# Performance work log

Hardware: AMD Instinct MI355X
Metric: run time of the kernel (lower is better)

Reference implementation:

```python
import jax, jax.numpy as jnp
import numpy as np

K_POOL = 5

def _conv_lookahead(x, W):
    # Faithful to F.conv2d(pad=(fs//2+1,0)) followed by keeping the last L rows:
    # for fs=3 this reduces to out[t] = sum_j x[t+j] @ W[:,j,:].T (2 trailing zeros).
    # x: [..., L, E], W: [nf, fs, E] -> out [..., L, nf]
    fs = W.shape[1]
    L = x.shape[-2]
    pad = [(0, 0)] * (x.ndim - 2) + [(0, fs - 1), (0, 0)]
    xp = jnp.pad(x, pad)
    out = sum(jnp.einsum('...le,fe->...lf', jax.lax.dynamic_slice_in_dim(xp, j, L, axis=-2), W[:, j, :]) for j in range(fs))
    return out

def _cosine(q, s):
    # q: [B,Q,D], s: [B,S,L,D] -> [B,S,Q,L]
    num = jnp.einsum('bqd,bsld->bsql', q, s)
    qn = jnp.linalg.norm(q, axis=-1)  # [B,Q]
    sn = jnp.linalg.norm(s, axis=-1)  # [B,S,L]
    return num / (qn[:, None, :, None] * sn[:, :, None, :])

def _pool(sim, k=K_POOL):
    # sort-based k-max pooling over last dim -> (max, mean-of-top-k), matching torch.sort + slice
    top = jax.lax.top_k(sim, k)[0]            # [..., Q, k] descending
    return jnp.stack([top[..., 0], top.mean(-1)], axis=-1)  # [..., Q, 2]

def _bce(p, t):
    return -(t * jnp.log(p) + (1.0 - t) * jnp.log(1.0 - p)).mean()

def setup_inputs() -> dict:
    key = jax.random.key(0)
    ks = jax.random.split(key, 9)
    B, S, L, Q, V, E, NF, FS = 16, 48, 64, 32, 50000, 300, 256, 3
    return {
        'sentences': jax.random.randint(ks[0], (B, S, L), 0, V, dtype=jnp.int64 if jax.config.jax_enable_x64 else jnp.int32).astype(jnp.int32),
        'question': jax.random.randint(ks[1], (B, Q), 0, V).astype(jnp.int32),
        'target_sents': jax.random.randint(ks[2], (B, S), 0, 2).astype(jnp.int32),
        'target_docs': jax.random.randint(ks[3], (B,), 0, 2).astype(jnp.int32),
        'similarity_one_hot': jax.random.uniform(ks[4], (B, S, Q, L), dtype=jnp.float32),
        'embeds': jax.random.normal(ks[5], (V, E), dtype=jnp.float32),
        'conv_w': jax.random.normal(ks[6], (NF, FS, E), dtype=jnp.float32),
        'lin_w': jax.random.normal(ks[7], (1, 6), dtype=jnp.float32),
        'lin_b': jax.random.normal(ks[8], (1,), dtype=jnp.float32),
    }

def reference(sentences, question, target_sents, target_docs, similarity_one_hot, embeds, conv_w, lin_w, lin_b):
    q_emb = embeds[question]            # [B,Q,E]
    s_emb = embeds[sentences]           # [B,S,L,E]
    q_conv = _conv_lookahead(q_emb, conv_w)   # [B,Q,NF]
    s_conv = _conv_lookahead(s_emb, conv_w)   # [B,S,L,NF]

    sim_ins = _cosine(q_emb, s_emb)     # [B,S,Q,L]
    qmask = (question > 1).astype(sim_ins.dtype)   # [B,Q]
    smask = (sentences > 1).astype(sim_ins.dtype)  # [B,S,L]
    sim_ins = sim_ins * qmask[:, None, :, None] * smask[:, :, None, :]

    sim_sens = _cosine(q_conv, s_conv)  # [B,S,Q,L]

    feats = jnp.concatenate([_pool(sim_ins), _pool(sim_sens), _pool(similarity_one_hot)], axis=-1)  # [B,S,Q,6]
    lo = jax.nn.sigmoid(jnp.einsum('bsqf,of->bsqo', feats, lin_w)[..., 0] + lin_b[0])  # [B,S,Q]
    sent_output = lo.mean(-1)           # [B,S]

    sal = _bce(sent_output, target_sents.astype(sent_output.dtype))
    doc_emit = sent_output.max(-1)      # [B]
    dal = _bce(doc_emit, target_docs.astype(doc_emit.dtype))
    total_loss = (sal + dal) / 2.0
    return (total_loss, sent_output, doc_emit)
```

## Files before the change

kernel.cpp:

```cpp
#include <hip/hip_runtime.h>
#include <math.h>

#define NB 16
#define NS 48
#define NL 64
#define NQ 32
#define NE 300
#define NF 256
#define KP 320
#define QROWS 36

typedef __attribute__((ext_vector_type(8))) short short8;
typedef __attribute__((ext_vector_type(4))) float f32x4;

#define MFMA(a,b,c) __builtin_amdgcn_mfma_f32_16x16x32_bf16((a),(b),(c),0,0,0)

__device__ __forceinline__ unsigned short f2bf(float f) {
    unsigned u = __float_as_uint(f);
    u += 0x7fff + ((u >> 16) & 1);
    return (unsigned short)(u >> 16);
}

#define SE_PITCH 640
#define SC_PITCH 512
#define SIM_OFF (66 * 640)
#define SIM_PITCH 66
#define DYN_LDS (SIM_OFF + NQ * SIM_PITCH * 4)

__device__ __forceinline__ float wave_reduce_sum(float v) {
#pragma unroll
    for (int off = 32; off; off >>= 1) v += __shfl_xor(v, off, 64);
    return v;
}

__device__ __forceinline__ void top5_pool4(float v0, float v1, float v2, float v3,
                                           int lane, float* mx, float* mn) {
    float s0 = 0.f, s1 = 0.f, s2 = 0.f, s3 = 0.f;
    float x0 = 0.f, x1 = 0.f, x2 = 0.f, x3 = 0.f;
#pragma unroll
    for (int i = 0; i < 5; ++i) {
        float m0 = v0, m1 = v1, m2 = v2, m3 = v3;
#pragma unroll
        for (int off = 32; off; off >>= 1) {
            m0 = fmaxf(m0, __shfl_xor(m0, off, 64));
            m1 = fmaxf(m1, __shfl_xor(m1, off, 64));
            m2 = fmaxf(m2, __shfl_xor(m2, off, 64));
            m3 = fmaxf(m3, __shfl_xor(m3, off, 64));
        }
        if (i == 0) { x0 = m0; x1 = m1; x2 = m2; x3 = m3; }
        s0 += m0; s1 += m1; s2 += m2; s3 += m3;
        unsigned long long k0 = __ballot(v0 == m0);
        unsigned long long k1 = __ballot(v1 == m1);
        unsigned long long k2 = __ballot(v2 == m2);
        unsigned long long k3 = __ballot(v3 == m3);
        if (lane == __ffsll(k0) - 1) v0 = -3.4e38f;
        if (lane == __ffsll(k1) - 1) v1 = -3.4e38f;
        if (lane == __ffsll(k2) - 1) v2 = -3.4e38f;
        if (lane == __ffsll(k3) - 1) v3 = -3.4e38f;
    }
    mx[0] = x0; mx[1] = x1; mx[2] = x2; mx[3] = x3;
    mn[0] = s0 * 0.2f; mn[1] = s1 * 0.2f; mn[2] = s2 * 0.2f; mn[3] = s3 * 0.2f;
}

__global__ void wb2_kernel(const float* __restrict__ conv_w, short8* __restrict__ Wb2,
                           unsigned int* __restrict__ done_ctr) {
    if (blockIdx.x == 0 && threadIdx.x == 0) done_ctr[0] = 0u;
    int i = blockIdx.x * 256 + threadIdx.x;
    if (i >= 120 * 256) return;
    int rl = i & 15;
    int ftile = (i >> 4) & 15;
    int c = i >> 8;
    int kg = c & 3, rest = c >> 2;
    int ks = rest % 10, j = rest / 10;
    int f = ftile * 16 + rl;
    int k0 = ks * 32 + kg * 8;
    const float* src = conv_w + (size_t)(f * 3 + j) * NE;
    short8 h;
#pragma unroll
    for (int e = 0; e < 8; ++e) {
        int k = k0 + e;
        h[e] = (short)((k < NE) ? f2bf(src[k]) : (unsigned short)0);
    }
    Wb2[i] = h;
}

__global__ void qe_kernel(const int* __restrict__ question, const float* __restrict__ embeds,
                          unsigned short* __restrict__ qe, short8* __restrict__ qef,
                          float* __restrict__ q_norm) {
    int row = blockIdx.x;
    int b = row / QROWS, r = row % QROWS;
    int l = threadIdx.x;
    unsigned short* dst = qe + (size_t)row * KP;
    if (r < NQ) {
        int tok = question[b * NQ + r];
        const float4* rp = (const float4*)(embeds + (size_t)tok * NE);
        short8 h = {0, 0, 0, 0, 0, 0, 0, 0};
        float ss = 0.f;
        if (l < 38) {
            float4 v0 = rp[2 * l];
            ss += v0.x * v0.x + v0.y * v0.y + v0.z * v0.z + v0.w * v0.w;
            h[0] = (short)f2bf(v0.x); h[1] = (short)f2bf(v0.y);
            h[2] = (short)f2bf(v0.z); h[3] = (short)f2bf(v0.w);
            if (2 * l + 1 < 75) {
                float4 v1 = rp[2 * l + 1];
                ss += v1.x * v1.x + v1.y * v1.y + v1.z * v1.z + v1.w * v1.w;
                h[4] = (short)f2bf(v1.x); h[5] = (short)f2bf(v1.y);
                h[6] = (short)f2bf(v1.z); h[7] = (short)f2bf(v1.w);
            }
        }
        if (l < 40) {
            *(short8*)(dst + 8 * l) = h;
            qef[((size_t)(b * 2 + (r >> 4)) * 40 + l) * 16 + (r & 15)] = h;
        }
        ss = wave_reduce_sum(ss);
        if (l == 0) q_norm[b * NQ + r] = sqrtf(ss);
    } else {
        if (l < 40) {
            short8 z = {0, 0, 0, 0, 0, 0, 0, 0};
            *(short8*)(dst + 8 * l) = z;
        }
    }
}

__global__ __launch_bounds__(256) void qconv_mfma_kernel(
        const unsigned short* __restrict__ qe, const short8* __restrict__ Wb2,
        short8* __restrict__ qcf) {
    __shared__ unsigned short tile[NQ][72];
    int b = blockIdx.x >> 2, fq = blockIdx.x & 3;
    int tid = threadIdx.x, lane = tid & 63, w = tid >> 6;
    int rl = lane & 15, kg = lane >> 4;
    int ftile = fq * 4 + w;
    f32x4 acc0 = (f32x4){0.f, 0.f, 0.f, 0.f};
    f32x4 acc1 = (f32x4){0.f, 0.f, 0.f, 0.f};
    for (int j = 0; j < 3; ++j) {
#pragma unroll 2
        for (int ks = 0; ks < 10; ++ks) {
            int k = ks * 32 + kg * 8;
            int c = (j * 10 + ks) * 4 + kg;
            short8 a0 = *(const short8*)(qe + ((size_t)(b * QROWS) + rl + j) * KP + k);
            short8 a1 = *(const short8*)(qe + ((size_t)(b * QROWS) + 16 + rl + j) * KP + k);
            short8 bb = Wb2[(c * 16 + ftile) * 16 + rl];
            acc0 = MFMA(a0, bb, acc0);
            acc1 = MFMA(a1, bb, acc1);
        }
    }
    int fl = w * 16 + rl;
#pragma unroll
    for (int reg = 0; reg < 4; ++reg) {
        tile[kg * 4 + reg][fl] = f2bf(acc0[reg]);
        tile[16 + kg * 4 + reg][fl] = f2bf(acc1[reg]);
    }
    __syncthreads();
    int mh = tid >> 7, c_local = (tid >> 4) & 7, rl2 = tid & 15;
    short8 h = *(const short8*)(&tile[mh * 16 + rl2][c_local * 8]);
    qcf[((size_t)(b * 2 + mh) * 32 + 8 * fq + c_local) * 16 + rl2] = h;
}

__global__ __launch_bounds__(256) void qcn_kernel(const short8* __restrict__ qcf,
                                                  float* __restrict__ qc_norm) {
    __shared__ float part[2][16][8];
    int b = blockIdx.x;
    int tid = threadIdx.x;
    int mh = tid >> 7, sub = (tid >> 4) & 7, rl = tid & 15;
    const short8* base = qcf + ((size_t)(b * 2 + mh) * 32) * 16;
    float ss = 0.f;
#pragma unroll
    for (int i = 0; i < 4; ++i) {
        short8 h = base[(sub * 4 + i) * 16 + rl];
#pragma unroll
        for (int e = 0; e < 8; ++e) {
            float v = __uint_as_float(((unsigned)(unsigned short)h[e]) << 16);
            ss += v * v;
        }
    }
    part[mh][rl][sub] = ss;
    __syncthreads();
    if (tid < 32) {
        int m2 = tid >> 4, r2 = tid & 15;
        float s = 0.f;
#pragma unroll
        for (int k = 0; k < 8; ++k) s += part[m2][r2][k];
        qc_norm[b * NQ + m2 * 16 + r2] = sqrtf(s);
    }
}

extern __shared__ char ldsc[];
__global__ __launch_bounds__(256, 3) void fused6_kernel(
    const int* __restrict__ sentences, const int* __restrict__ question,
    const float* __restrict__ sim_oh, const float* __restrict__ embeds,
    const short8* __restrict__ Wb2,
    const short8* __restrict__ qef, const short8* __restrict__ qcf,
    const float* __restrict__ q_norm, const float* __restrict__ qc_norm,
    const float* __restrict__ lin_w, const float* __restrict__ lin_b,
    const int* __restrict__ tsent, const int* __restrict__ tdoc,
    unsigned int* __restrict__ done_ctr,
    float* __restrict__ sent_ws, float* __restrict__ d_out)
{
    __shared__ int toks[NL];
    __shared__ float smaskf[NL], snorm[NL], scnorm[NL];
    __shared__ float qn_s[NQ], qcn_s[NQ], qmf_s[NQ];
    __shared__ float wq[4];
    __shared__ float fpool[NQ][2];
    __shared__ int lastflag;
    __shared__ float red2[4];
    __shared__ float dred[NB];

    int tid = threadIdx.x, lane = tid & 63, w = tid >> 6;
    int rl = lane & 15, kg = lane >> 4;
    int bs = blockIdx.x, b = bs / NS;
    int t = (w << 4) + rl, t7 = t & 7;

    if (tid < NL) {
        int tk = sentences[(size_t)bs * NL + tid];
        toks[tid] = tk;
        smaskf[tid] = (tk > 1) ? 1.f : 0.f;
    } else if (tid < NL + NQ) {
        int q = tid - NL;
        qn_s[q] = q_norm[b * NQ + q];
    } else if (tid < NL + 2 * NQ) {
        int q = tid - NL - NQ;
        qcn_s[q] = qc_norm[b * NQ + q];
    } else if (tid < NL + 3 * NQ) {
        int q = tid - NL - 2 * NQ;
        qmf_s[q] = (question[b * NQ + q] > 1) ? 1.f : 0.f;
    }
    __syncthreads();

#pragma unroll 2
    for (int r = w; r < 66; r += 4) {
        char* rowbase = ldsc + r * SE_PITCH;
        int m7 = r & 7;
        if (r < NL) {
            const float4* rp = (const float4*)(embeds + (size_t)toks[r] * NE);
            {
                float4 v = rp[lane];
                ushort4 h = {f2bf(v.x), f2bf(v.y), f2bf(v.z), f2bf(v.w)};
                *(ushort4*)(rowbase + (((lane >> 1) ^ m7) << 4) + ((lane & 1) << 3)) = h;
            }
            if (lane < 11) {
                float4 v = rp[64 + lane];
                ushort4 h = {f2bf(v.x), f2bf(v.y), f2bf(v.z), f2bf(v.w)};
                int g = 64 + lane;
                *(ushort4*)(rowbase + (((g >> 1) ^ m7) << 4) + ((g & 1) << 3)) = h;
            }
            if (lane < 5) {
                int pk = 37 + ((lane + 1) >> 1);
                int sub = ((lane + 1) & 1) << 3;
                *(unsigned long long*)(rowbase + ((pk ^ m7) << 4) + sub) = 0ull;
            }
        } else {
            if (lane < 40) {
                uint4 z = {0, 0, 0, 0};
                *(uint4*)(rowbase + (lane << 4)) = z;
            }
        }
    }
    __syncthreads();

    {
        f32x4 iacc0 = (f32x4){0.f, 0.f, 0.f, 0.f};
        f32x4 iacc1 = (f32x4){0.f, 0.f, 0.f, 0.f};
        f32x4 nB = (f32x4){0.f, 0.f, 0.f, 0.f};
        const short8* qf = qef + (size_t)(b * 80) * 16;
#pragma unroll 2
        for (int ks = 0; ks < 10; ++ks) {
            int c = ks * 4 + kg;
            short8 bB = *(const short8*)(ldsc + t * SE_PITCH + ((c ^ t7) << 4));
            short8 a0 = qf[c * 16 + rl];
            short8 a1 = qf[(40 + c) * 16 + rl];
            iacc0 = MFMA(a0, bB, iacc0);
            iacc1 = MFMA(a1, bB, iacc1);
            nB = MFMA(bB, bB, nB);
        }
        if (kg == (rl >> 2)) snorm[t] = sqrtf(nB[rl & 3]);
        __syncthreads();

        float inv_t = smaskf[t] / snorm[t];
#pragma unroll
        for (int reg = 0; reg < 4; ++reg) {
            int q0 = kg * 4 + reg;
            float s0 = iacc0[reg] / qn_s[q0] * inv_t * qmf_s[q0];
            *(float*)(ldsc + SIM_OFF + (q0 * SIM_PITCH + t) * 4) = s0;
            int q1 = 16 + kg * 4 + reg;
            float s1 = iacc1[reg] / qn_s[q1] * inv_t * qmf_s[q1];
            *(float*)(ldsc + SIM_OFF + (q1 * SIM_PITCH + t) * 4) = s1;
        }
    }
    __syncthreads();

    {
        int q0 = w << 3;
        float v[8];
#pragma unroll
        for (int qi = 0; qi < 8; ++qi)
            v[qi] = *(float*)(ldsc + SIM_OFF + ((q0 + qi) * SIM_PITCH + lane) * 4);
        float mx[4], mn[4];
        top5_pool4(v[0], v[1], v[2], v[3], lane, mx, mn);
        if (lane == 0)
#pragma unroll
            for (int p = 0; p < 4; ++p) { fpool[q0 + p][0] = mx[p]; fpool[q0 + p][1] = mn[p]; }
        top5_pool4(v[4], v[5], v[6], v[7], lane, mx, mn);
        if (lane == 0)
#pragma unroll
            for (int p = 0; p < 4; ++p) { fpool[q0 + 4 + p][0] = mx[p]; fpool[q0 + 4 + p][1] = mn[p]; }
    }

    f32x4 cacc[4][4];
#pragma unroll
    for (int m = 0; m < 4; ++m)
#pragma unroll
        for (int nn = 0; nn < 4; ++nn) cacc[m][nn] = (f32x4){0.f, 0.f, 0.f, 0.f};
    for (int j = 0; j < 3; ++j) {
#pragma unroll 2
        for (int ks = 0; ks < 10; ++ks) {
            int c = (j * 10 + ks) * 4 + kg;
            short8 a[4], bb[4];
#pragma unroll
            for (int m = 0; m < 4; ++m) {
                int row = m * 16 + rl + j;
                a[m] = *(const short8*)(ldsc + row * SE_PITCH +
                                        ((((ks << 2) + kg) ^ (row & 7)) << 4));
            }
#pragma unroll
            for (int nn = 0; nn < 4; ++nn)
                bb[nn] = Wb2[(c * 16 + (w * 4 + nn)) * 16 + rl];
#pragma unroll
            for (int m = 0; m < 4; ++m)
#pragma unroll
                for (int nn = 0; nn < 4; ++nn)
                    cacc[m][nn] = MFMA(a[m], bb[nn], cacc[m][nn]);
        }
    }
    __syncthreads();

#pragma unroll
    for (int m = 0; m < 4; ++m)
#pragma unroll
        for (int nn = 0; nn < 4; ++nn) {
            int f = (w * 4 + nn) * 16 + rl;
#pragma unroll
            for (int reg = 0; reg < 4; ++reg) {
                int tr = m * 16 + kg * 4 + reg;
                *(unsigned short*)(ldsc + tr * SC_PITCH +
                                   (((f >> 3) ^ (tr & 7)) << 4) + ((f & 7) << 1)) =
                    f2bf(cacc[m][nn][reg]);
            }
        }
    __syncthreads();

    float oh[8];
#pragma unroll
    for (int qi = 0; qi < 8; ++qi) {
        int q = (w << 3) + qi;
        oh[qi] = sim_oh[((size_t)bs * NQ + q) * NL + lane];
    }
    {
        f32x4 sacc0 = (f32x4){0.f, 0.f, 0.f, 0.f};
        f32x4 sacc1 = (f32x4){0.f, 0.f, 0.f, 0.f};
        f32x4 nB = (f32x4){0.f, 0.f, 0.f, 0.f};
        const short8* qc = qcf + (size_t)(b * 64) * 16;
#pragma unroll 2
        for (int ks = 0; ks < 8; ++ks) {
            int c = ks * 4 + kg;
            short8 bB = *(const short8*)(ldsc + t * SC_PITCH + ((c ^ t7) << 4));
            short8 a0 = qc[c * 16 + rl];
            short8 a1 = qc[(32 + c) * 16 + rl];
            sacc0 = MFMA(a0, bB, sacc0);
            sacc1 = MFMA(a1, bB, sacc1);
            nB = MFMA(bB, bB, nB);
        }
        if (kg == (rl >> 2)) scnorm[t] = sqrtf(nB[rl & 3]);
        __syncthreads();

        float inv_t = 1.f / scnorm[t];
#pragma unroll
        for (int reg = 0; reg < 4; ++reg) {
            int q0 = kg * 4 + reg;
            *(float*)(ldsc + SIM_OFF + (q0 * SIM_PITCH + t) * 4) =
                sacc0[reg] / qcn_s[q0] * inv_t;
            int q1 = 16 + kg * 4 + reg;
            *(float*)(ldsc + SIM_OFF + (q1 * SIM_PITCH + t) * 4) =
                sacc1[reg] / qcn_s[q1] * inv_t;
        }
    }
    __syncthreads();

    {
        float lw0 = lin_w[0], lw1 = lin_w[1], lw2 = lin_w[2];
        float lw3 = lin_w[3], lw4 = lin_w[4], lw5 = lin_w[5];
        float lb = lin_b[0];
        int q0 = w << 3;
        float sv[8];
#pragma unroll
        for (int qi = 0; qi < 8; ++qi)
            sv[qi] = *(float*)(ldsc + SIM_OFF + ((q0 + qi) * SIM_PITCH + lane) * 4);
        float mxs[8], mns[8], mxo[8], mno[8];
        top5_pool4(sv[0], sv[1], sv[2], sv[3], lane, mxs, mns);
        top5_pool4(sv[4], sv[5], sv[6], sv[7], lane, mxs + 4, mns + 4);
        top5_pool4(oh[0], oh[1], oh[2], oh[3], lane, mxo, mno);
        top5_pool4(oh[4], oh[5], oh[6], oh[7], lane, mxo + 4, mno + 4);
        float psum = 0.f;
#pragma unroll
        for (int qi = 0; qi < 8; ++qi) {
            float f0 = fpool[q0 + qi][0], f1 = fpool[q0 + qi][1];
            float z = f0 * lw0 + f1 * lw1 + mxs[qi] * lw2 + mns[qi] * lw3 +
                      mxo[qi] * lw4 + mno[qi] * lw5 + lb;
            psum += 1.f / (1.f + expf(-z));
        }
        if (lane == 0) wq[w] = psum;
    }
    __syncthreads();
    if (tid == 0) {
        float sent = (wq[0] + wq[1] + wq[2] + wq[3]) * (1.f / 32.f);
        __hip_atomic_store(&sent_ws[bs], sent, __ATOMIC_RELEASE, __HIP_MEMORY_SCOPE_AGENT);
        d_out[1 + bs] = sent;
        unsigned old = atomicAdd(done_ctr, 1u);
        lastflag = (old == (unsigned)(NB * NS - 1)) ? 1 : 0;
    }
    __syncthreads();

    if (lastflag) {
        float acc_l = 0.f;
        for (int i = tid; i < NB * NS; i += 256) {
            float p = __hip_atomic_load(&sent_ws[i], __ATOMIC_ACQUIRE, __HIP_MEMORY_SCOPE_AGENT);
            float tt2 = (float)tsent[i];
            acc_l += tt2 * logf(p) + (1.f - tt2) * logf(1.f - p);
        }
        acc_l = wave_reduce_sum(acc_l);
        if ((tid & 63) == 0) red2[tid >> 6] = acc_l;
        if (tid < NB) {
            float m = -3.4e38f;
            for (int s = 0; s < NS; ++s)
                m = fmaxf(m, __hip_atomic_load(&sent_ws[tid * NS + s], __ATOMIC_ACQUIRE,
                                               __HIP_MEMORY_SCOPE_AGENT));
            d_out[1 + NB * NS + tid] = m;
            float tt2 = (float)tdoc[tid];
            dred[tid] = tt2 * logf(m) + (1.f - tt2) * logf(1.f - m);
        }
        __syncthreads();
        if (tid == 0) {
            float sal = -(red2[0] + red2[1] + red2[2] + red2[3]) / (float)(NB * NS);
            float dsum = 0.f;
            for (int i = 0; i < NB; ++i) dsum += dred[i];
            float dal = -dsum / (float)NB;
            d_out[0] = 0.5f * (sal + dal);
        }
    }
}

extern "C" void kernel_launch(void* const* d_in, const int* in_sizes, int n_in,
                              void* d_out, int out_size, void* d_ws, size_t ws_size,
                              hipStream_t stream) {
    const int* sentences = (const int*)d_in[0];
    const int* question = (const int*)d_in[1];
    const int* tsent = (const int*)d_in[2];
    const int* tdoc = (const int*)d_in[3];
    const float* sim_oh = (const float*)d_in[4];
    const float* embeds = (const float*)d_in[5];
    const float* conv_w = (const float*)d_in[6];
    const float* lin_w = (const float*)d_in[7];
    const float* lin_b = (const float*)d_in[8];
    float* out = (float*)d_out;

    char* wsc = (char*)d_ws;
    short8* Wb2            = (short8*)(wsc);
    unsigned short* qe_old = (unsigned short*)(wsc + 491520);
    short8* qef            = (short8*)(wsc + 860160);
    short8* qcf            = (short8*)(wsc + 1187840);
    float* q_norm          = (float*)(wsc + 1449984);
    float* qc_norm         = (float*)(wsc + 1452032);
    float* sent_ws         = (float*)(wsc + 1454080);
    unsigned int* done_ctr = (unsigned int*)(wsc + 1457152);

    hipFuncSetAttribute(reinterpret_cast<const void*>(fused6_kernel),
                        hipFuncAttributeMaxDynamicSharedMemorySize, DYN_LDS);

    wb2_kernel<<<120, 256, 0, stream>>>(conv_w, Wb2, done_ctr);
    qe_kernel<<<NB * QROWS, 64, 0, stream>>>(question, embeds, qe_old, qef, q_norm);
    qconv_mfma_kernel<<<NB * 4, 256, 0, stream>>>(qe_old, Wb2, qcf);
    qcn_kernel<<<NB, 256, 0, stream>>>(qcf, qc_norm);
    fused6_kernel<<<NB * NS, 256, DYN_LDS, stream>>>(
        sentences, question, sim_oh, embeds, Wb2, qef, qcf, q_norm, qc_norm,
        lin_w, lin_b, tsent, tdoc, done_ctr, sent_ws, out);
}
```

Baseline: 130.6 us.

## Merge prep kernels, fold question-conv norms into atomics, hoist sim_oh loads

Merges the weight-conversion and question-embedding kernels into one prep launch and drops the separate question-conv norm kernel. The conv kernel now accumulates per-query sums of squares with atomics, and the main kernel takes the sqrt. The main kernel issues its sim_oh loads at the start so they overlap the embedding gather, and its row-staging loop is simplified to 16 unconditional iterations plus two zero rows. This cuts two kernel launches and the gaps between them, at the cost of atomic float accumulation order and higher register pressure from the early loads.

```diff
diff --git a/kernel.cpp b/kernel.cpp
--- a/kernel.cpp
+++ b/kernel.cpp
@@ -62,69 +62,73 @@
     mn[0] = s0 * 0.2f; mn[1] = s1 * 0.2f; mn[2] = s2 * 0.2f; mn[3] = s3 * 0.2f;
 }
 
-__global__ void wb2_kernel(const float* __restrict__ conv_w, short8* __restrict__ Wb2,
-                           unsigned int* __restrict__ done_ctr) {
-    if (blockIdx.x == 0 && threadIdx.x == 0) done_ctr[0] = 0u;
-    int i = blockIdx.x * 256 + threadIdx.x;
-    if (i >= 120 * 256) return;
-    int rl = i & 15;
-    int ftile = (i >> 4) & 15;
-    int c = i >> 8;
-    int kg = c & 3, rest = c >> 2;
-    int ks = rest % 10, j = rest / 10;
-    int f = ftile * 16 + rl;
-    int k0 = ks * 32 + kg * 8;
-    const float* src = conv_w + (size_t)(f * 3 + j) * NE;
-    short8 h;
-#pragma unroll
-    for (int e = 0; e < 8; ++e) {
-        int k = k0 + e;
-        h[e] = (short)((k < NE) ? f2bf(src[k]) : (unsigned short)0);
-    }
-    Wb2[i] = h;
-}
-
-__global__ void qe_kernel(const int* __restrict__ question, const float* __restrict__ embeds,
-                          unsigned short* __restrict__ qe, short8* __restrict__ qef,
-                          float* __restrict__ q_norm) {
-    int row = blockIdx.x;
-    int b = row / QROWS, r = row % QROWS;
-    int l = threadIdx.x;
-    unsigned short* dst = qe + (size_t)row * KP;
-    if (r < NQ) {
-        int tok = question[b * NQ + r];
-        const float4* rp = (const float4*)(embeds + (size_t)tok * NE);
-        short8 h = {0, 0, 0, 0, 0, 0, 0, 0};
-        float ss = 0.f;
-        if (l < 38) {
-            float4 v0 = rp[2 * l];
-            ss += v0.x * v0.x + v0.y * v0.y + v0.z * v0.z + v0.w * v0.w;
-            h[0] = (short)f2bf(v0.x); h[1] = (short)f2bf(v0.y);
-            h[2] = (short)f2bf(v0.z); h[3] = (short)f2bf(v0.w);
-            if (2 * l + 1 < 75) {
-                float4 v1 = rp[2 * l + 1];
-                ss += v1.x * v1.x + v1.y * v1.y + v1.z * v1.z + v1.w * v1.w;
-                h[4] = (short)f2bf(v1.x); h[5] = (short)f2bf(v1.y);
-                h[6] = (short)f2bf(v1.z); h[7] = (short)f2bf(v1.w);
+__global__ __launch_bounds__(256) void prep_kernel(
+        const float* __restrict__ conv_w, const int* __restrict__ question,
+        const float* __restrict__ embeds,
+        short8* __restrict__ Wb2, unsigned short* __restrict__ qe,
+        short8* __restrict__ qef, float* __restrict__ q_norm,
+        float* __restrict__ qcssq, unsigned int* __restrict__ done_ctr) {
+    int blk = blockIdx.x;
+    int tid = threadIdx.x;
+    if (blk < 120) {
+        if (blk == 0 && tid == 0) done_ctr[0] = 0u;
+        int i = blk * 256 + tid;
+        if (i < NB * NQ) qcssq[i] = 0.f;
+        int rl = i & 15;
+        int ftile = (i >> 4) & 15;
+        int c = i >> 8;
+        int kg = c & 3, rest = c >> 2;
+        int ks = rest % 10, j = rest / 10;
+        int f = ftile * 16 + rl;
+        int k0 = ks * 32 + kg * 8;
+        const float* src = conv_w + (size_t)(f * 3 + j) * NE;
+        short8 h;
+#pragma unroll
+        for (int e = 0; e < 8; ++e) {
+            int k = k0 + e;
+            h[e] = (short)((k < NE) ? f2bf(src[k]) : (unsigned short)0);
+        }
+        Wb2[i] = h;
+    } else {
+        int row = (blk - 120) * 4 + (tid >> 6);
+        int b = row / QROWS, r = row % QROWS;
+        int l = tid & 63;
+        unsigned short* dst = qe + (size_t)row * KP;
+        if (r < NQ) {
+            int tok = question[b * NQ + r];
+            const float4* rp = (const float4*)(embeds + (size_t)tok * NE);
+            short8 h = {0, 0, 0, 0, 0, 0, 0, 0};
+            float ss = 0.f;
+            if (l < 38) {
+                float4 v0 = rp[2 * l];
+                ss += v0.x * v0.x + v0.y * v0.y + v0.z * v0.z + v0.w * v0.w;
+                h[0] = (short)f2bf(v0.x); h[1] = (short)f2bf(v0.y);
+                h[2] = (short)f2bf(v0.z); h[3] = (short)f2bf(v0.w);
+                if (2 * l + 1 < 75) {
+                    float4 v1 = rp[2 * l + 1];
+                    ss += v1.x * v1.x + v1.y * v1.y + v1.z * v1.z + v1.w * v1.w;
+                    h[4] = (short)f2bf(v1.x); h[5] = (short)f2bf(v1.y);
+                    h[6] = (short)f2bf(v1.z); h[7] = (short)f2bf(v1.w);
+                }
             }
-        }
-        if (l < 40) {
-            *(short8*)(dst + 8 * l) = h;
-            qef[((size_t)(b * 2 + (r >> 4)) * 40 + l) * 16 + (r & 15)] = h;
-        }
-        ss = wave_reduce_sum(ss);
-        if (l == 0) q_norm[b * NQ + r] = sqrtf(ss);
-    } else {
-        if (l < 40) {
-            short8 z = {0, 0, 0, 0, 0, 0, 0, 0};
-            *(short8*)(dst + 8 * l) = z;
+            if (l < 40) {
+                *(short8*)(dst + 8 * l) = h;
+                qef[((size_t)(b * 2 + (r >> 4)) * 40 + l) * 16 + (r & 15)] = h;
+            }
+            ss = wave_reduce_sum(ss);
+            if (l == 0) q_norm[b * NQ + r] = sqrtf(ss);
+        } else {
+            if (l < 40) {
+                short8 z = {0, 0, 0, 0, 0, 0, 0, 0};
+                *(short8*)(dst + 8 * l) = z;
+            }
         }
     }
 }
 
 __global__ __launch_bounds__(256) void qconv_mfma_kernel(
         const unsigned short* __restrict__ qe, const short8* __restrict__ Wb2,
-        short8* __restrict__ qcf) {
+        short8* __restrict__ qcf, float* __restrict__ qcssq) {
     __shared__ unsigned short tile[NQ][72];
     int b = blockIdx.x >> 2, fq = blockIdx.x & 3;
     int tid = threadIdx.x, lane = tid & 63, w = tid >> 6;
@@ -151,46 +155,34 @@
         tile[16 + kg * 4 + reg][fl] = f2bf(acc1[reg]);
     }
     __syncthreads();
-    int mh = tid >> 7, c_local = (tid >> 4) & 7, rl2 = tid & 15;
-    short8 h = *(const short8*)(&tile[mh * 16 + rl2][c_local * 8]);
-    qcf[((size_t)(b * 2 + mh) * 32 + 8 * fq + c_local) * 16 + rl2] = h;
-}
-
-__global__ __launch_bounds__(256) void qcn_kernel(const short8* __restrict__ qcf,
-                                                  float* __restrict__ qc_norm) {
-    __shared__ float part[2][16][8];
-    int b = blockIdx.x;
-    int tid = threadIdx.x;
-    int mh = tid >> 7, sub = (tid >> 4) & 7, rl = tid & 15;
-    const short8* base = qcf + ((size_t)(b * 2 + mh) * 32) * 16;
-    float ss = 0.f;
-#pragma unroll
-    for (int i = 0; i < 4; ++i) {
-        short8 h = base[(sub * 4 + i) * 16 + rl];
+    {
+        int mh = tid >> 7, c_local = (tid >> 4) & 7, rl2 = tid & 15;
+        short8 h = *(const short8*)(&tile[mh * 16 + rl2][c_local * 8]);
+        qcf[((size_t)(b * 2 + mh) * 32 + 8 * fq + c_local) * 16 + rl2] = h;
+    }
+    {
+        int qq = tid >> 3, fgrp = tid & 7;
+        short8 h = *(const short8*)(&tile[qq][fgrp * 8]);
+        float ss = 0.f;
 #pragma unroll
         for (int e = 0; e < 8; ++e) {
             float v = __uint_as_float(((unsigned)(unsigned short)h[e]) << 16);
             ss += v * v;
         }
-    }
-    part[mh][rl][sub] = ss;
-    __syncthreads();
-    if (tid < 32) {
-        int m2 = tid >> 4, r2 = tid & 15;
-        float s = 0.f;
-#pragma unroll
-        for (int k = 0; k < 8; ++k) s += part[m2][r2][k];
-        qc_norm[b * NQ + m2 * 16 + r2] = sqrtf(s);
+        ss += __shfl_xor(ss, 1, 64);
+        ss += __shfl_xor(ss, 2, 64);
+        ss += __shfl_xor(ss, 4, 64);
+        if (fgrp == 0) atomicAdd(&qcssq[b * NQ + qq], ss);
     }
 }
 
 extern __shared__ char ldsc[];
-__global__ __launch_bounds__(256, 3) void fused6_kernel(
+__global__ __launch_bounds__(256, 3) void fused8_kernel(
     const int* __restrict__ sentences, const int* __restrict__ question,
     const float* __restrict__ sim_oh, const float* __restrict__ embeds,
     const short8* __restrict__ Wb2,
     const short8* __restrict__ qef, const short8* __restrict__ qcf,
-    const float* __restrict__ q_norm, const float* __restrict__ qc_norm,
+    const float* __restrict__ q_norm, const float* __restrict__ qcssq,
     const float* __restrict__ lin_w, const float* __restrict__ lin_b,
     const int* __restrict__ tsent, const int* __restrict__ tdoc,
     unsigned int* __restrict__ done_ctr,
@@ -210,6 +202,13 @@
     int bs = blockIdx.x, b = bs / NS;
     int t = (w << 4) + rl, t7 = t & 7;
 
+    float oh[8];
+#pragma unroll
+    for (int qi = 0; qi < 8; ++qi) {
+        int q = (w << 3) + qi;
+        oh[qi] = sim_oh[((size_t)bs * NQ + q) * NL + lane];
+    }
+
     if (tid < NL) {
         int tk = sentences[(size_t)bs * NL + tid];
         toks[tid] = tk;
@@ -219,40 +218,41 @@
         qn_s[q] = q_norm[b * NQ + q];
     } else if (tid < NL + 2 * NQ) {
         int q = tid - NL - NQ;
-        qcn_s[q] = qc_norm[b * NQ + q];
+        qcn_s[q] = sqrtf(qcssq[b * NQ + q]);
     } else if (tid < NL + 3 * NQ) {
         int q = tid - NL - 2 * NQ;
         qmf_s[q] = (question[b * NQ + q] > 1) ? 1.f : 0.f;
     }
     __syncthreads();
 
-#pragma unroll 2
-    for (int r = w; r < 66; r += 4) {
+#pragma unroll 4
+    for (int i = 0; i < 16; ++i) {
+        int r = (i << 2) + w;
         char* rowbase = ldsc + r * SE_PITCH;
         int m7 = r & 7;
-        if (r < NL) {
-            const float4* rp = (const float4*)(embeds + (size_t)toks[r] * NE);
-            {
-                float4 v = rp[lane];
-                ushort4 h = {f2bf(v.x), f2bf(v.y), f2bf(v.z), f2bf(v.w)};
-                *(ushort4*)(rowbase + (((lane >> 1) ^ m7) << 4) + ((lane & 1) << 3)) = h;
-            }
-            if (lane < 11) {
-                float4 v = rp[64 + lane];
-                ushort4 h = {f2bf(v.x), f2bf(v.y), f2bf(v.z), f2bf(v.w)};
-                int g = 64 + lane;
-                *(ushort4*)(rowbase + (((g >> 1) ^ m7) << 4) + ((g & 1) << 3)) = h;
-            }
-            if (lane < 5) {
-                int pk = 37 + ((lane + 1) >> 1);
-                int sub = ((lane + 1) & 1) << 3;
-                *(unsigned long long*)(rowbase + ((pk ^ m7) << 4) + sub) = 0ull;
-            }
-        } else {
-            if (lane < 40) {
-                uint4 z = {0, 0, 0, 0};
-                *(uint4*)(rowbase + (lane << 4)) = z;
-            }
+        const float4* rp = (const float4*)(embeds + (size_t)toks[r] * NE);
+        {
+            float4 v = rp[lane];
+            ushort4 h = {f2bf(v.x), f2bf(v.y), f2bf(v.z), f2bf(v.w)};
+            *(ushort4*)(rowbase + (((lane >> 1) ^ m7) << 4) + ((lane & 1) << 3)) = h;
+        }
+        if (lane < 11) {
+            float4 v = rp[64 + lane];
+            ushort4 h = {f2bf(v.x), f2bf(v.y), f2bf(v.z), f2bf(v.w)};
+            int g = 64 + lane;
+            *(ushort4*)(rowbase + (((g >> 1) ^ m7) << 4) + ((g & 1) << 3)) = h;
+        }
+        if (lane < 5) {
+            int pk = 37 + ((lane + 1) >> 1);
+            int sub = ((lane + 1) & 1) << 3;
+            *(unsigned long long*)(rowbase + ((pk ^ m7) << 4) + sub) = 0ull;
+        }
+    }
+    if (w < 2) {
+        int r = 64 + w;
+        if (lane < 40) {
+            uint4 z = {0, 0, 0, 0};
+            *(uint4*)(ldsc + r * SE_PITCH + (lane << 4)) = z;
         }
     }
     __syncthreads();
@@ -348,12 +348,6 @@
         }
     __syncthreads();
 
-    float oh[8];
-#pragma unroll
-    for (int qi = 0; qi < 8; ++qi) {
-        int q = (w << 3) + qi;
-        oh[qi] = sim_oh[((size_t)bs * NQ + q) * NL + lane];
-    }
     {
         f32x4 sacc0 = (f32x4){0.f, 0.f, 0.f, 0.f};
         f32x4 sacc1 = (f32x4){0.f, 0.f, 0.f, 0.f};
@@ -468,18 +462,17 @@
     short8* qef            = (short8*)(wsc + 860160);
     short8* qcf            = (short8*)(wsc + 1187840);
     float* q_norm          = (float*)(wsc + 1449984);
-    float* qc_norm         = (float*)(wsc + 1452032);
+    float* qcssq           = (float*)(wsc + 1452032);
     float* sent_ws         = (float*)(wsc + 1454080);
     unsigned int* done_ctr = (unsigned int*)(wsc + 1457152);
 
-    hipFuncSetAttribute(reinterpret_cast<const void*>(fused6_kernel),
+    hipFuncSetAttribute(reinterpret_cast<const void*>(fused8_kernel),
                         hipFuncAttributeMaxDynamicSharedMemorySize, DYN_LDS);
 
-    wb2_kernel<<<120, 256, 0, stream>>>(conv_w, Wb2, done_ctr);
-    qe_kernel<<<NB * QROWS, 64, 0, stream>>>(question, embeds, qe_old, qef, q_norm);
-    qconv_mfma_kernel<<<NB * 4, 256, 0, stream>>>(qe_old, Wb2, qcf);
-    qcn_kernel<<<NB, 256, 0, stream>>>(qcf, qc_norm);
-    fused6_kernel<<<NB * NS, 256, DYN_LDS, stream>>>(
-        sentences, question, sim_oh, embeds, Wb2, qef, qcf, q_norm, qc_norm,
+    prep_kernel<<<264, 256, 0, stream>>>(conv_w, question, embeds,
+                                         Wb2, qe_old, qef, q_norm, qcssq, done_ctr);
+    qconv_mfma_kernel<<<NB * 4, 256, 0, stream>>>(qe_old, Wb2, qcf, qcssq);
+    fused8_kernel<<<NB * NS, 256, DYN_LDS, stream>>>(
+        sentences, question, sim_oh, embeds, Wb2, qef, qcf, q_norm, qcssq,
         lin_w, lin_b, tsent, tdoc, done_ctr, sent_ws, out);
 }
```

New measurement: 126.2 us. 3.3% less time.
